# Kernel optimization log

Hardware: AMD Instinct MI355X
Metric: run time of the kernel (lower is better)

The kernel has to match this reference:

```python
import jax, jax.numpy as jnp
import numpy as np

T, B, D, H, S = 512, 32, 1024, 1024, 512


def setup_inputs() -> dict:
    key = jax.random.key(0)
    ks = jax.random.split(key, 10)
    sc = 0.02
    return {
        "x": jax.random.normal(ks[0], (T, B, D), jnp.float32),
        "h0": jax.random.normal(ks[1], (B, H), jnp.float32),
        "c0": jax.random.normal(ks[2], (B, H), jnp.float32),
        "ctx": jax.random.normal(ks[3], (S, B, H), jnp.float32),
        # nn.Linear(input_size, 4*hidden_size) with bias
        "W_ih": jax.random.normal(ks[4], (4 * H, D), jnp.float32) * sc,
        "b_ih": jax.random.normal(ks[5], (4 * H,), jnp.float32) * sc,
        # nn.Linear(hidden_size, 4*hidden_size) with bias
        "W_hh": jax.random.normal(ks[6], (4 * H, H), jnp.float32) * sc,
        "b_hh": jax.random.normal(ks[7], (4 * H,), jnp.float32) * sc,
        # SoftDotAttention: linear_in (H->H, no bias), linear_out (2H->H, no bias)
        "W_in": jax.random.normal(ks[8], (H, H), jnp.float32) * sc,
        "W_out": jax.random.normal(ks[9], (H, 2 * H), jnp.float32) * sc,
    }


def reference(x, h0, c0, ctx, W_ih, b_ih, W_hh, b_hh, W_in, W_out):
    ctx_b = jnp.swapaxes(ctx, 0, 1)  # [B, S, H] (ctx.transpose(0,1))

    def step(carry, xt):
        hx, cx = carry
        gates = xt @ W_ih.T + b_ih + hx @ W_hh.T + b_hh  # [B, 4H]
        i, f, g, o = jnp.split(gates, 4, axis=1)
        cy = jax.nn.sigmoid(f) * cx + jax.nn.sigmoid(i) * jnp.tanh(g)
        hy = jax.nn.sigmoid(o) * jnp.tanh(cy)  # [B, H]
        # SoftDotAttention
        target = hy @ W_in.T  # [B, H]
        attn = jax.nn.softmax(jnp.einsum("bsh,bh->bs", ctx_b, target), axis=-1)
        wc = jnp.einsum("bs,bsh->bh", attn, ctx_b)  # weighted context
        h_tilde = jnp.tanh(jnp.concatenate([wc, hy], axis=1) @ W_out.T)
        return (h_tilde, cy), h_tilde

    (hT, cT), out = jax.lax.scan(step, (h0, c0), x)
    return out, hT, cT
```

## Files before the change

### kernel.cpp

```cpp
#include <hip/hip_runtime.h>
#include <hip/hip_bf16.h>
#include <cstdint>
#include <cstddef>

#define TT 512
#define BB 32
#define DD 1024
#define HH 1024
#define SS 512

typedef _Float16 f16x8 __attribute__((ext_vector_type(8)));
typedef _Float16 f16x4 __attribute__((ext_vector_type(4)));
typedef _Float16 f16x2 __attribute__((ext_vector_type(2)));
typedef float f32x4 __attribute__((ext_vector_type(4)));

__device__ __forceinline__ float sigm(float x) { return 1.0f / (1.0f + __expf(-x)); }
__device__ __forceinline__ float tanh_fast(float x) {
    return 1.0f - 2.0f / (__expf(2.0f * x) + 1.0f);
}
__device__ __forceinline__ f16x8 cvt8(const float* __restrict__ p) {
    float4 u = *(const float4*)p;
    float4 v = *(const float4*)(p + 4);
    f16x8 r;
    r[0] = (_Float16)u.x; r[1] = (_Float16)u.y; r[2] = (_Float16)u.z; r[3] = (_Float16)u.w;
    r[4] = (_Float16)v.x; r[5] = (_Float16)v.y; r[6] = (_Float16)v.z; r[7] = (_Float16)v.w;
    return r;
}

__device__ __forceinline__ void st_u32_coh(unsigned* p, unsigned v) {
    __hip_atomic_store(p, v, __ATOMIC_RELAXED, __HIP_MEMORY_SCOPE_AGENT);
}
__device__ __forceinline__ unsigned ld_u32_coh(const unsigned* p) {
    return __hip_atomic_load(p, __ATOMIC_RELAXED, __HIP_MEMORY_SCOPE_AGENT);
}
__device__ __forceinline__ f16x8 ld16_coh(const _Float16* p) {
    union { unsigned long long q[2]; f16x8 h; } u;
    u.q[0] = __hip_atomic_load((const unsigned long long*)p, __ATOMIC_RELAXED,
                               __HIP_MEMORY_SCOPE_AGENT);
    u.q[1] = __hip_atomic_load((const unsigned long long*)p + 1, __ATOMIC_RELAXED,
                               __HIP_MEMORY_SCOPE_AGENT);
    return u.h;
}

__global__ __launch_bounds__(256) void k_cvt(const float* __restrict__ s,
                                             _Float16* __restrict__ d, int n4) {
    for (int i = blockIdx.x * blockDim.x + threadIdx.x; i < n4; i += gridDim.x * blockDim.x) {
        float4 v = ((const float4*)s)[i];
        f16x4 h;
        h[0] = (_Float16)v.x; h[1] = (_Float16)v.y;
        h[2] = (_Float16)v.z; h[3] = (_Float16)v.w;
        ((f16x4*)d)[i] = h;
    }
}

__global__ void k_bias(const float* __restrict__ bih, const float* __restrict__ bhh,
                       float* __restrict__ bsum) {
    const int i = blockIdx.x * blockDim.x + threadIdx.x;
    if (i < 4 * HH) bsum[i] = bih[i] + bhh[i];
}

__global__ void k_init(const float* __restrict__ c0, float* __restrict__ cbuf) {
    const int i = blockIdx.x * blockDim.x + threadIdx.x;
    if (i < BB * HH) cbuf[i] = c0[i];
}

__global__ void k_zero(unsigned* __restrict__ p) {
    const int i = blockIdx.x * blockDim.x + threadIdx.x;
    if (i < 1024) p[i] = 0u;
}

__global__ void k_fin(const float* __restrict__ lasth, const float* __restrict__ cbuf,
                      float* __restrict__ hT, float* __restrict__ cT) {
    const int i = blockIdx.x * blockDim.x + threadIdx.x;
    if (i < BB * HH) {
        hT[i] = lasth[i];
        cT[i] = cbuf[i];
    }
}

__global__ __launch_bounds__(256) void k_pre(const float* __restrict__ x,
                                             const float* __restrict__ Wih,
                                             _Float16* __restrict__ gx) {
    const int wave = (blockIdx.x * blockDim.x + threadIdx.x) >> 6;
    const int lane = threadIdx.x & 63;
    const int m0 = (wave >> 6) * 64, n0 = (wave & 63) * 64;
    const int lm = lane & 15, q8 = (lane >> 4) * 8;

    f32x4 acc[4][4];
    #pragma unroll
    for (int i = 0; i < 4; ++i)
        #pragma unroll
        for (int j = 0; j < 4; ++j) acc[i][j] = (f32x4)0.0f;

    for (int k0 = 0; k0 < DD; k0 += 32) {
        f16x8 a[4], b[4];
        #pragma unroll
        for (int i = 0; i < 4; ++i)
            a[i] = cvt8(x + (size_t)(m0 + i * 16 + lm) * DD + k0 + q8);
        #pragma unroll
        for (int j = 0; j < 4; ++j)
            b[j] = cvt8(Wih + (size_t)(n0 + j * 16 + lm) * DD + k0 + q8);
        #pragma unroll
        for (int i = 0; i < 4; ++i)
            #pragma unroll
            for (int j = 0; j < 4; ++j)
                acc[i][j] = __builtin_amdgcn_mfma_f32_16x16x32_f16(a[i], b[j], acc[i][j], 0, 0, 0);
    }
    const int rq = (lane >> 4) * 4;
    #pragma unroll
    for (int i = 0; i < 4; ++i)
        #pragma unroll
        for (int j = 0; j < 4; ++j)
            #pragma unroll
            for (int r = 0; r < 4; ++r)
                gx[(size_t)(m0 + i * 16 + rq + r) * (4 * HH) + n0 + j * 16 + lm] =
                    (_Float16)acc[i][j][r];
}

__global__ __launch_bounds__(256) void k_trwin(const float* __restrict__ Win,
                                               _Float16* __restrict__ WinT) {
    __shared__ float tile[32][33];
    const int bx = blockIdx.x & 31, by = blockIdx.x >> 5;
    const int tx = threadIdx.x & 31, ty = threadIdx.x >> 5;
    #pragma unroll
    for (int r = 0; r < 4; ++r)
        tile[ty + r * 8][tx] = Win[(size_t)(by * 32 + ty + r * 8) * HH + bx * 32 + tx];
    __syncthreads();
    #pragma unroll
    for (int r = 0; r < 4; ++r)
        WinT[(size_t)(bx * 32 + ty + r * 8) * HH + by * 32 + tx] =
            (_Float16)tile[tx][ty + r * 8];
}

__global__ __launch_bounds__(256) void k_ctxw(const float* __restrict__ ctxf,
                                              const _Float16* __restrict__ WinT,
                                              _Float16* __restrict__ ctxW) {
    const int wave = (blockIdx.x * blockDim.x + threadIdx.x) >> 6;
    const int lane = threadIdx.x & 63;
    const int m0 = (wave >> 4) * 64, n0 = (wave & 15) * 64;
    const int lm = lane & 15, q8 = (lane >> 4) * 8;

    f32x4 acc[4][4];
    #pragma unroll
    for (int i = 0; i < 4; ++i)
        #pragma unroll
        for (int j = 0; j < 4; ++j) acc[i][j] = (f32x4)0.0f;

    for (int k0 = 0; k0 < HH; k0 += 32) {
        f16x8 a[4], b[4];
        #pragma unroll
        for (int i = 0; i < 4; ++i)
            a[i] = cvt8(ctxf + (size_t)(m0 + i * 16 + lm) * HH + k0 + q8);
        #pragma unroll
        for (int j = 0; j < 4; ++j)
            b[j] = *(const f16x8*)(WinT + (size_t)(n0 + j * 16 + lm) * HH + k0 + q8);
        #pragma unroll
        for (int i = 0; i < 4; ++i)
            #pragma unroll
            for (int j = 0; j < 4; ++j)
                acc[i][j] = __builtin_amdgcn_mfma_f32_16x16x32_f16(a[i], b[j], acc[i][j], 0, 0, 0);
    }
    const int rq = (lane >> 4) * 4;
    #pragma unroll
    for (int i = 0; i < 4; ++i)
        #pragma unroll
        for (int j = 0; j < 4; ++j)
            #pragma unroll
            for (int r = 0; r < 4; ++r)
                ctxW[(size_t)(m0 + i * 16 + rq + r) * HH + n0 + j * 16 + lm] =
                    (_Float16)acc[i][j][r];
}

__device__ __forceinline__ void gbar4(unsigned* __restrict__ flags, unsigned round) {
    __syncthreads();
    const int tid = threadIdx.x;
    if (tid == 0) {
        asm volatile("s_waitcnt vmcnt(0)" ::: "memory");
        st_u32_coh(&flags[blockIdx.x], round);
    }
    if (tid < 64) {
        int guard = 0;
        for (;;) {
            const unsigned a0 = ld_u32_coh(&flags[tid * 4 + 0]);
            const unsigned a1 = ld_u32_coh(&flags[tid * 4 + 1]);
            const unsigned a2 = ld_u32_coh(&flags[tid * 4 + 2]);
            const unsigned a3 = ld_u32_coh(&flags[tid * 4 + 3]);
            if (a0 >= round && a1 >= round && a2 >= round && a3 >= round) break;
            __builtin_amdgcn_s_sleep(1);
            if (++guard > (1 << 20)) break;
        }
    }
    __syncthreads();
}

__global__ __launch_bounds__(512, 1) void k_persist(
    const _Float16* __restrict__ x16,
    const _Float16* __restrict__ ctx_h,
    const _Float16* __restrict__ ctxW,
    const float* __restrict__ Whh,
    const float* __restrict__ Wih,
    const float* __restrict__ Wout,
    const float* __restrict__ bsum,
    float* __restrict__ cbuf,
    _Float16* __restrict__ h16,
    _Float16* __restrict__ hy16,
    _Float16* __restrict__ wc16,
    float* __restrict__ scores,
    float* __restrict__ out,
    unsigned* __restrict__ bar) {
    __shared__ __align__(16) _Float16 sWHH[16 * 1024];
    __shared__ __align__(16) _Float16 sWIH[16 * 1024];
    __shared__ __align__(16) _Float16 sWOUT[4 * 2048];
    __shared__ __align__(16) float sRED[4096];
    __shared__ float sSM[512];

    const int bid = blockIdx.x;
    const int tid = threadIdx.x;
    const int w = tid >> 6, lane = tid & 63;
    const int lm = lane & 15, q8 = (lane >> 4) * 8;
    const int j0 = bid * 4;

    for (int idx = tid; idx < 16 * 128; idx += 512) {
        const int p = idx >> 7, k8 = idx & 127;
        const int g = (p >> 2) * HH + j0 + (p & 3);
        const int dst = (p * 2048 + k8 * 16) ^ ((p & 7) << 4);
        *(f16x8*)((char*)sWHH + dst) = cvt8(Whh + (size_t)g * HH + k8 * 8);
        *(f16x8*)((char*)sWIH + dst) = cvt8(Wih + (size_t)g * DD + k8 * 8);
    }
    for (int idx = tid; idx < 4 * 256; idx += 512) {
        const int p = idx >> 8, k8 = idx & 255;
        *(f16x8*)((char*)sWOUT + ((p * 4096 + k8 * 16) ^ (p << 4))) =
            cvt8(Wout + (size_t)(j0 + p) * (2 * HH) + k8 * 8);
    }
    __syncthreads();

    unsigned round = 0;
    for (int t = 0; t < TT; ++t) {
        {
            const int kb = (w & 3) * 256;
            f32x4 acc0 = (f32x4)0.0f, acc1 = (f32x4)0.0f;
            if (w < 4) {
                #pragma unroll
                for (int kk = 0; kk < 256; kk += 32) {
                    const int k0 = kb + kk + q8;
                    f16x8 a0 = ld16_coh(h16 + (size_t)lm * HH + k0);
                    f16x8 a1 = ld16_coh(h16 + (size_t)(16 + lm) * HH + k0);
                    f16x8 bb = *(const f16x8*)((const char*)sWHH +
                                 ((lm * 2048 + k0 * 2) ^ ((lm & 7) << 4)));
                    acc0 = __builtin_amdgcn_mfma_f32_16x16x32_f16(a0, bb, acc0, 0, 0, 0);
                    acc1 = __builtin_amdgcn_mfma_f32_16x16x32_f16(a1, bb, acc1, 0, 0, 0);
                }
            } else {
                const _Float16* Xb = x16 + (size_t)t * (BB * DD);
                #pragma unroll
                for (int kk = 0; kk < 256; kk += 32) {
                    const int k0 = kb + kk + q8;
                    f16x8 a0 = *(const f16x8*)(Xb + (size_t)lm * DD + k0);
                    f16x8 a1 = *(const f16x8*)(Xb + (size_t)(16 + lm) * DD + k0);
                    f16x8 bb = *(const f16x8*)((const char*)sWIH +
                                 ((lm * 2048 + k0 * 2) ^ ((lm & 7) << 4)));
                    acc0 = __builtin_amdgcn_mfma_f32_16x16x32_f16(a0, bb, acc0, 0, 0, 0);
                    acc1 = __builtin_amdgcn_mfma_f32_16x16x32_f16(a1, bb, acc1, 0, 0, 0);
                }
            }
            ((f32x4*)sRED)[(w * 2 + 0) * 64 + lane] = acc0;
            ((f32x4*)sRED)[(w * 2 + 1) * 64 + lane] = acc1;
            __syncthreads();
            {
                const int b = tid >> 4, p = tid & 15;
                const int mt = b >> 4, bi = b & 15;
                const int ln = ((bi >> 2) << 4) | p, r = bi & 3;
                float gv = 0.0f;
                #pragma unroll
                for (int w2 = 0; w2 < 8; ++w2)
                    gv += sRED[((w2 * 2 + mt) * 64 + ln) * 4 + r];
                sSM[tid] = gv;
            }
            __syncthreads();
            if (tid < 64) {
                const int b = tid >> 1, cp = (tid & 1) * 2;
                union { _Float16 h[2]; unsigned u; } pk;
                #pragma unroll
                for (int cc = 0; cc < 2; ++cc) {
                    const int c = cp + cc, j = j0 + c;
                    const float gi = sSM[b * 16 + 0 + c] + bsum[j];
                    const float gf = sSM[b * 16 + 4 + c] + bsum[HH + j];
                    const float gg = sSM[b * 16 + 8 + c] + bsum[2 * HH + j];
                    const float go = sSM[b * 16 + 12 + c] + bsum[3 * HH + j];
                    const float cprev = cbuf[b * HH + j];
                    const float cy = sigm(gf) * cprev + sigm(gi) * tanh_fast(gg);
                    const float hv = sigm(go) * tanh_fast(cy);
                    cbuf[b * HH + j] = cy;
                    pk.h[cc] = (_Float16)hv;
                }
                st_u32_coh((unsigned*)(hy16 + (size_t)b * HH + j0 + cp), pk.u);
            }
        }
        ++round;
        gbar4(bar, round);

        {
            const int b = bid & 31, s0 = (bid >> 5) * 64;
            const _Float16* hrow = hy16 + (size_t)b * HH + lane * 16;
            const f16x8 hv0 = ld16_coh(hrow);
            const f16x8 hv1 = ld16_coh(hrow + 8);
            float hf[16];
            #pragma unroll
            for (int i = 0; i < 8; ++i) { hf[i] = (float)hv0[i]; hf[8 + i] = (float)hv1[i]; }
            #pragma unroll
            for (int i = 0; i < 8; ++i) {
                const int s = s0 + w * 8 + i;
                const _Float16* crow = ctxW + ((size_t)s * BB + b) * HH + lane * 16;
                const f16x8 c0 = *(const f16x8*)(crow);
                const f16x8 c1 = *(const f16x8*)(crow + 8);
                float sum = 0.0f;
                #pragma unroll
                for (int jj = 0; jj < 8; ++jj)
                    sum += hf[jj] * (float)c0[jj] + hf[8 + jj] * (float)c1[jj];
                #pragma unroll
                for (int off = 32; off > 0; off >>= 1) sum += __shfl_down(sum, off, 64);
                if (lane == 0)
                    st_u32_coh((unsigned*)(scores + b * SS + s), __float_as_uint(sum));
            }
        }
        ++round;
        gbar4(bar, round);

        {
            const int b = bid >> 3, h0 = (bid & 7) * 128;
            const float v = __uint_as_float(ld_u32_coh((const unsigned*)(scores + b * SS + tid)));
            float mx = v;
            #pragma unroll
            for (int off = 32; off > 0; off >>= 1) mx = fmaxf(mx, __shfl_xor(mx, off, 64));
            if (lane == 0) sRED[w] = mx;
            __syncthreads();
            mx = sRED[0];
            #pragma unroll
            for (int w2 = 1; w2 < 8; ++w2) mx = fmaxf(mx, sRED[w2]);
            const float e = __expf(v - mx);
            sSM[tid] = e;
            float ssum = e;
            #pragma unroll
            for (int off = 32; off > 0; off >>= 1) ssum += __shfl_xor(ssum, off, 64);
            if (lane == 0) sRED[8 + w] = ssum;
            __syncthreads();
            float tot = 0.0f;
            #pragma unroll
            for (int w2 = 0; w2 < 8; ++w2) tot += sRED[8 + w2];
            const float inv = 1.0f / tot;
            float a0 = 0.0f, a1 = 0.0f;
            const _Float16* cb = ctx_h + ((size_t)(w * 64) * BB + b) * HH + h0 + lane * 2;
            #pragma unroll 16
            for (int i = 0; i < 64; ++i) {
                const float aw = sSM[w * 64 + i];
                const f16x2 u = *(const f16x2*)(cb + (size_t)i * (BB * HH));
                a0 += aw * (float)u[0];
                a1 += aw * (float)u[1];
            }
            __syncthreads();
            sRED[(w * 64 + lane) * 2 + 0] = a0;
            sRED[(w * 64 + lane) * 2 + 1] = a1;
            __syncthreads();
            if (tid < 64) {
                const int ln = tid;
                float sv0 = 0.0f, sv1 = 0.0f;
                #pragma unroll
                for (int w2 = 0; w2 < 8; ++w2) {
                    sv0 += sRED[(w2 * 64 + ln) * 2 + 0];
                    sv1 += sRED[(w2 * 64 + ln) * 2 + 1];
                }
                union { _Float16 h[2]; unsigned u; } pk;
                pk.h[0] = (_Float16)(sv0 * inv);
                pk.h[1] = (_Float16)(sv1 * inv);
                st_u32_coh((unsigned*)(wc16 + (size_t)b * HH + h0 + ln * 2), pk.u);
            }
        }
        ++round;
        gbar4(bar, round);

        {
            const _Float16* Ab = (w < 4) ? wc16 : hy16;
            const int kb = (w & 3) * 256;
            const int koff = (w < 4) ? 0 : HH;
            const int pc = lm & 3;
            f32x4 acc0 = (f32x4)0.0f, acc1 = (f32x4)0.0f;
            #pragma unroll
            for (int kk = 0; kk < 256; kk += 32) {
                const int k0 = kb + kk + q8;
                f16x8 a0 = ld16_coh(Ab + (size_t)lm * HH + k0);
                f16x8 a1 = ld16_coh(Ab + (size_t)(16 + lm) * HH + k0);
                f16x8 bb = *(const f16x8*)((char*)sWOUT +
                             ((pc * 4096 + (koff + k0) * 2) ^ (pc << 4)));
                acc0 = __builtin_amdgcn_mfma_f32_16x16x32_f16(a0, bb, acc0, 0, 0, 0);
                acc1 = __builtin_amdgcn_mfma_f32_16x16x32_f16(a1, bb, acc1, 0, 0, 0);
            }
            ((f32x4*)sRED)[(w * 2 + 0) * 64 + lane] = acc0;
            ((f32x4*)sRED)[(w * 2 + 1) * 64 + lane] = acc1;
            __syncthreads();
            {
                const int b = tid >> 4, p = tid & 15;
                const int mt = b >> 4, bi = b & 15;
                const int ln = ((bi >> 2) << 4) | p, r = bi & 3;
                float v2 = 0.0f;
                #pragma unroll
                for (int w2 = 0; w2 < 8; ++w2)
                    v2 += sRED[((w2 * 2 + mt) * 64 + ln) * 4 + r];
                const float ht = tanh_fast(v2);
                if (p < 4) out[(size_t)t * (BB * HH) + b * HH + j0 + p] = ht;
                sSM[tid] = ht;
            }
            __syncthreads();
            if (tid < 64) {
                const int b2 = tid >> 1, pp = (tid & 1) * 2;
                union { _Float16 h[2]; unsigned u; } pk;
                pk.h[0] = (_Float16)sSM[b2 * 16 + pp];
                pk.h[1] = (_Float16)sSM[b2 * 16 + pp + 1];
                st_u32_coh((unsigned*)(h16 + (size_t)b2 * HH + j0 + pp), pk.u);
            }
        }
        ++round;
        gbar4(bar, round);
    }
}

__global__ __launch_bounds__(64) void k_step1(const float* __restrict__ hprev,
                                              const _Float16* __restrict__ Whh_h,
                                              const float* __restrict__ Whh_f,
                                              const _Float16* __restrict__ gx_t,
                                              const float* __restrict__ xt_f,
                                              const _Float16* __restrict__ Wih_h,
                                              const float* __restrict__ Wih_f,
                                              const float* __restrict__ bsum,
                                              float* __restrict__ cbuf,
                                              float* __restrict__ hy,
                                              int use_pre, int staged) {
    const int wave = blockIdx.x;
    const int lane = threadIdx.x;
    const int m0 = (wave >> 6) * 16;
    const int j0 = (wave & 63) * 16;
    const int lm = lane & 15, q8 = (lane >> 4) * 8;

    f32x4 acc[4];
    #pragma unroll
    for (int q = 0; q < 4; ++q) acc[q] = (f32x4)0.0f;

    const float* arow = hprev + (size_t)(m0 + lm) * HH;
    if (staged) {
        for (int k0 = 0; k0 < HH; k0 += 32) {
            f16x8 a = cvt8(arow + k0 + q8);
            #pragma unroll
            for (int q = 0; q < 4; ++q) {
                f16x8 b = *(const f16x8*)(Whh_h + (size_t)(q * HH + j0 + lm) * HH + k0 + q8);
                acc[q] = __builtin_amdgcn_mfma_f32_16x16x32_f16(a, b, acc[q], 0, 0, 0);
            }
        }
    } else {
        for (int k0 = 0; k0 < HH; k0 += 32) {
            f16x8 a = cvt8(arow + k0 + q8);
            #pragma unroll
            for (int q = 0; q < 4; ++q) {
                f16x8 b = cvt8(Whh_f + (size_t)(q * HH + j0 + lm) * HH + k0 + q8);
                acc[q] = __builtin_amdgcn_mfma_f32_16x16x32_f16(a, b, acc[q], 0, 0, 0);
            }
        }
    }
    if (!use_pre) {
        const float* xrow = xt_f + (size_t)(m0 + lm) * DD;
        if (staged) {
            for (int k0 = 0; k0 < DD; k0 += 32) {
                f16x8 a = cvt8(xrow + k0 + q8);
                #pragma unroll
                for (int q = 0; q < 4; ++q) {
                    f16x8 b = *(const f16x8*)(Wih_h + (size_t)(q * HH + j0 + lm) * DD + k0 + q8);
                    acc[q] = __builtin_amdgcn_mfma_f32_16x16x32_f16(a, b, acc[q], 0, 0, 0);
                }
            }
        } else {
            for (int k0 = 0; k0 < DD; k0 += 32) {
                f16x8 a = cvt8(xrow + k0 + q8);
                #pragma unroll
                for (int q = 0; q < 4; ++q) {
                    f16x8 b = cvt8(Wih_f + (size_t)(q * HH + j0 + lm) * DD + k0 + q8);
                    acc[q] = __builtin_amdgcn_mfma_f32_16x16x32_f16(a, b, acc[q], 0, 0, 0);
                }
            }
        }
    }
    const int rq = (lane >> 4) * 4;
    const int j = j0 + lm;
    const float bs_i = bsum[j], bs_f = bsum[HH + j], bs_g = bsum[2 * HH + j], bs_o = bsum[3 * HH + j];
    #pragma unroll
    for (int r = 0; r < 4; ++r) {
        const int b = m0 + rq + r;
        float gi = acc[0][r] + bs_i, gf = acc[1][r] + bs_f;
        float gg = acc[2][r] + bs_g, go = acc[3][r] + bs_o;
        if (use_pre) {
            const _Float16* g = gx_t + (size_t)b * (4 * HH);
            gi += (float)g[j];
            gf += (float)g[HH + j];
            gg += (float)g[2 * HH + j];
            go += (float)g[3 * HH + j];
        }
        const float cprev = cbuf[b * HH + j];
        const float cy = sigm(gf) * cprev + sigm(gi) * tanh_fast(gg);
        const float hv = sigm(go) * tanh_fast(cy);
        cbuf[b * HH + j] = cy;
        hy[b * HH + j] = hv;
    }
}

__global__ __launch_bounds__(64) void k_target(const float* __restrict__ hy,
                                               const _Float16* __restrict__ Win_h,
                                               const float* __restrict__ Win_f,
                                               float* __restrict__ target,
                                               int staged) {
    const int wave = blockIdx.x;
    const int lane = threadIdx.x;
    const int m0 = (wave >> 6) * 16;
    const int j0 = (wave & 63) * 16;
    const int lm = lane & 15, q8 = (lane >> 4) * 8;

    f32x4 acc = (f32x4)0.0f;
    const float* arow = hy + (size_t)(m0 + lm) * HH;
    if (staged) {
        for (int k0 = 0; k0 < HH; k0 += 32) {
            f16x8 a = cvt8(arow + k0 + q8);
            f16x8 b = *(const f16x8*)(Win_h + (size_t)(j0 + lm) * HH + k0 + q8);
            acc = __builtin_amdgcn_mfma_f32_16x16x32_f16(a, b, acc, 0, 0, 0);
        }
    } else {
        for (int k0 = 0; k0 < HH; k0 += 32) {
            f16x8 a = cvt8(arow + k0 + q8);
            f16x8 b = cvt8(Win_f + (size_t)(j0 + lm) * HH + k0 + q8);
            acc = __builtin_amdgcn_mfma_f32_16x16x32_f16(a, b, acc, 0, 0, 0);
        }
    }
    const int rq = (lane >> 4) * 4;
    const int j = j0 + lm;
    #pragma unroll
    for (int r = 0; r < 4; ++r)
        target[(m0 + rq + r) * HH + j] = acc[r];
}

__global__ __launch_bounds__(256) void k_scores(const _Float16* __restrict__ ctx_h,
                                                const float* __restrict__ ctx_f,
                                                const float* __restrict__ target,
                                                float* __restrict__ scores, int staged) {
    const int idx = (blockIdx.x * blockDim.x + threadIdx.x) >> 6;
    const int lane = threadIdx.x & 63;
    const int b = idx >> 9;
    const int s = idx & 511;
    const float* trow = target + b * HH + lane * 16;
    float4 t0 = *(const float4*)(trow);
    float4 t1 = *(const float4*)(trow + 4);
    float4 t2 = *(const float4*)(trow + 8);
    float4 t3 = *(const float4*)(trow + 12);
    float sum = 0.0f;
    if (staged) {
        const _Float16* crow = ctx_h + ((size_t)s * BB + b) * HH + lane * 16;
        f16x8 c0 = *(const f16x8*)(crow);
        f16x8 c1 = *(const f16x8*)(crow + 8);
        sum += (float)c0[0] * t0.x + (float)c0[1] * t0.y + (float)c0[2] * t0.z + (float)c0[3] * t0.w;
        sum += (float)c0[4] * t1.x + (float)c0[5] * t1.y + (float)c0[6] * t1.z + (float)c0[7] * t1.w;
        sum += (float)c1[0] * t2.x + (float)c1[1] * t2.y + (float)c1[2] * t2.z + (float)c1[3] * t2.w;
        sum += (float)c1[4] * t3.x + (float)c1[5] * t3.y + (float)c1[6] * t3.z + (float)c1[7] * t3.w;
    } else {
        const float* crow = ctx_f + ((size_t)s * BB + b) * HH + lane * 16;
        float4 c0 = *(const float4*)(crow);
        float4 c1 = *(const float4*)(crow + 4);
        float4 c2 = *(const float4*)(crow + 8);
        float4 c3 = *(const float4*)(crow + 12);
        sum += c0.x * t0.x + c0.y * t0.y + c0.z * t0.z + c0.w * t0.w;
        sum += c1.x * t1.x + c1.y * t1.y + c1.z * t1.z + c1.w * t1.w;
        sum += c2.x * t2.x + c2.y * t2.y + c2.z * t2.z + c2.w * t2.w;
        sum += c3.x * t3.x + c3.y * t3.y + c3.z * t3.z + c3.w * t3.w;
    }
    #pragma unroll
    for (int off = 32; off > 0; off >>= 1) sum += __shfl_down(sum, off, 64);
    if (lane == 0) scores[b * SS + s] = sum;
}

__global__ __launch_bounds__(256) void k_attn(const _Float16* __restrict__ ctx_h,
                                              const float* __restrict__ ctx_f,
                                              const float* __restrict__ scores,
                                              float* __restrict__ wc, int staged) {
    __shared__ float sm[SS];
    __shared__ float red[256];
    const int b = blockIdx.x >> 1;
    const int hc = blockIdx.x & 1;
    const int t = threadIdx.x;

    const float v0 = scores[b * SS + t];
    const float v1 = scores[b * SS + 256 + t];
    red[t] = fmaxf(v0, v1);
    __syncthreads();
    for (int o = 128; o > 0; o >>= 1) {
        if (t < o) red[t] = fmaxf(red[t], red[t + o]);
        __syncthreads();
    }
    const float mx = red[0];
    __syncthreads();
    const float e0 = __expf(v0 - mx);
    const float e1 = __expf(v1 - mx);
    sm[t] = e0;
    sm[t + 256] = e1;
    red[t] = e0 + e1;
    __syncthreads();
    for (int o = 128; o > 0; o >>= 1) {
        if (t < o) red[t] += red[t + o];
        __syncthreads();
    }
    const float inv = 1.0f / red[0];

    const int h = hc * 512 + t * 2;
    float a0 = 0.0f, a1 = 0.0f;
    if (staged) {
        const _Float16* cbase = ctx_h + (size_t)b * HH + h;
        #pragma unroll 8
        for (int s = 0; s < SS; ++s) {
            const float a = sm[s];
            const f16x2 u = *(const f16x2*)(cbase + (size_t)s * (BB * HH));
            a0 += a * (float)u[0];
            a1 += a * (float)u[1];
        }
    } else {
        const float* cbase = ctx_f + (size_t)b * HH + h;
        #pragma unroll 8
        for (int s = 0; s < SS; ++s) {
            const float a = sm[s];
            const float2 u = *(const float2*)(cbase + (size_t)s * (BB * HH));
            a0 += a * u.x;
            a1 += a * u.y;
        }
    }
    wc[b * HH + h] = a0 * inv;
    wc[b * HH + h + 1] = a1 * inv;
}

__global__ __launch_bounds__(64) void k_out(const float* __restrict__ wc,
                                            const float* __restrict__ hy,
                                            const _Float16* __restrict__ Wout_h,
                                            const float* __restrict__ Wout_f,
                                            float* __restrict__ out_t,
                                            int staged) {
    const int wave = blockIdx.x;
    const int lane = threadIdx.x;
    const int m0 = (wave >> 6) * 16;
    const int j0 = (wave & 63) * 16;
    const int lm = lane & 15, q8 = (lane >> 4) * 8;

    f32x4 acc = (f32x4)0.0f;
    const float* arow1 = wc + (size_t)(m0 + lm) * HH;
    const float* arow2 = hy + (size_t)(m0 + lm) * HH;
    if (staged) {
        const _Float16* brow = Wout_h + (size_t)(j0 + lm) * (2 * HH);
        for (int k0 = 0; k0 < HH; k0 += 32) {
            f16x8 a = cvt8(arow1 + k0 + q8);
            f16x8 b = *(const f16x8*)(brow + k0 + q8);
            acc = __builtin_amdgcn_mfma_f32_16x16x32_f16(a, b, acc, 0, 0, 0);
        }
        for (int k0 = 0; k0 < HH; k0 += 32) {
            f16x8 a = cvt8(arow2 + k0 + q8);
            f16x8 b = *(const f16x8*)(brow + HH + k0 + q8);
            acc = __builtin_amdgcn_mfma_f32_16x16x32_f16(a, b, acc, 0, 0, 0);
        }
    } else {
        const float* brow = Wout_f + (size_t)(j0 + lm) * (2 * HH);
        for (int k0 = 0; k0 < HH; k0 += 32) {
            f16x8 a = cvt8(arow1 + k0 + q8);
            f16x8 b = cvt8(brow + k0 + q8);
            acc = __builtin_amdgcn_mfma_f32_16x16x32_f16(a, b, acc, 0, 0, 0);
        }
        for (int k0 = 0; k0 < HH; k0 += 32) {
            f16x8 a = cvt8(arow2 + k0 + q8);
            f16x8 b = cvt8(brow + HH + k0 + q8);
            acc = __builtin_amdgcn_mfma_f32_16x16x32_f16(a, b, acc, 0, 0, 0);
        }
    }
    const int rq = (lane >> 4) * 4;
    const int j = j0 + lm;
    #pragma unroll
    for (int r = 0; r < 4; ++r)
        out_t[(m0 + rq + r) * HH + j] = tanh_fast(acc[r]);
}

static constexpr size_t NW_CBUF   = 0;
static constexpr size_t NW_SCORES = 131072;
static constexpr size_t NW_HY16   = 196608;
static constexpr size_t NW_H16    = 262144;
static constexpr size_t NW_WC16   = 327680;
static constexpr size_t NW_BSUM   = 393216;
static constexpr size_t NW_BAR    = 409600;
static constexpr size_t NW_WINT   = 413696;
static constexpr size_t NW_X16    = 2510848;
static constexpr size_t NW_CTXH   = 36065280;
static constexpr size_t NW_CTXW   = 69619712;
static constexpr size_t NW_TOTAL  = 103174144;

extern "C" void kernel_launch(void* const* d_in, const int* in_sizes, int n_in,
                              void* d_out, int out_size, void* d_ws, size_t ws_size,
                              hipStream_t stream) {
    const float* x    = (const float*)d_in[0];
    const float* h0   = (const float*)d_in[1];
    const float* c0   = (const float*)d_in[2];
    const float* ctx  = (const float*)d_in[3];
    const float* Wih  = (const float*)d_in[4];
    const float* bih  = (const float*)d_in[5];
    const float* Whh  = (const float*)d_in[6];
    const float* bhh  = (const float*)d_in[7];
    const float* Win  = (const float*)d_in[8];
    const float* Wout = (const float*)d_in[9];
    float* out = (float*)d_out;
    char* ws = (char*)d_ws;

    if (ws_size >= NW_TOTAL) {
        float* cbuf       = (float*)(ws + NW_CBUF);
        float* scores     = (float*)(ws + NW_SCORES);
        _Float16* hy16    = (_Float16*)(ws + NW_HY16);
        _Float16* h16     = (_Float16*)(ws + NW_H16);
        _Float16* wc16    = (_Float16*)(ws + NW_WC16);
        float* bsum       = (float*)(ws + NW_BSUM);
        unsigned* bar     = (unsigned*)(ws + NW_BAR);
        _Float16* WinT    = (_Float16*)(ws + NW_WINT);
        _Float16* x16     = (_Float16*)(ws + NW_X16);
        _Float16* ctx_h   = (_Float16*)(ws + NW_CTXH);
        _Float16* ctxW    = (_Float16*)(ws + NW_CTXW);

        k_bias<<<16, 256, 0, stream>>>(bih, bhh, bsum);
        k_init<<<128, 256, 0, stream>>>(c0, cbuf);
        k_zero<<<4, 256, 0, stream>>>(bar);
        k_cvt<<<2048, 256, 0, stream>>>(ctx, ctx_h, SS * BB * HH / 4);
        k_cvt<<<4096, 256, 0, stream>>>(x, x16, TT * BB * DD / 4);
        k_cvt<<<32, 256, 0, stream>>>(h0, h16, BB * HH / 4);
        k_trwin<<<1024, 256, 0, stream>>>(Win, WinT);
        k_ctxw<<<1024, 256, 0, stream>>>(ctx, WinT, ctxW);

        k_persist<<<256, 512, 0, stream>>>(x16, ctx_h, ctxW, Whh, Wih, Wout, bsum,
                                           cbuf, h16, hy16, wc16, scores, out, bar);

        float* hT = out + (size_t)TT * BB * HH;
        float* cT = hT + BB * HH;
        k_fin<<<128, 256, 0, stream>>>(out + (size_t)(TT - 1) * BB * HH, cbuf, hT, cT);
        return;
    }

    float* cbuf   = (float*)(ws + 0);
    float* hy     = (float*)(ws + 131072);
    float* target = (float*)(ws + 262144);
    float* scores = (float*)(ws + 393216);
    float* wc     = (float*)(ws + 458752);
    float* bsum   = (float*)(ws + 589824);
    _Float16* Whh_h  = (_Float16*)(ws + 606208);
    _Float16* Win_h  = (_Float16*)(ws + 8994816);
    _Float16* Wout_h = (_Float16*)(ws + 11091968);
    _Float16* Wih_h  = (_Float16*)(ws + 15286272);
    _Float16* ctx_h  = (_Float16*)(ws + 23674880);
    _Float16* gx     = (_Float16*)(ws + 57229312);

    const int staged  = (ws_size >= (size_t)57229312) ? 1 : 0;
    const int use_pre = (ws_size >= (size_t)191447040) ? 1 : 0;

    k_bias<<<16, 256, 0, stream>>>(bih, bhh, bsum);
    k_init<<<128, 256, 0, stream>>>(c0, cbuf);
    if (staged) {
        k_cvt<<<1024, 256, 0, stream>>>(Whh, Whh_h, 4 * HH * HH / 4);
        k_cvt<<<1024, 256, 0, stream>>>(Win, Win_h, HH * HH / 4);
        k_cvt<<<1024, 256, 0, stream>>>(Wout, Wout_h, 2 * HH * HH / 4);
        k_cvt<<<2048, 256, 0, stream>>>(ctx, ctx_h, SS * BB * HH / 4);
        if (!use_pre) k_cvt<<<1024, 256, 0, stream>>>(Wih, Wih_h, 4 * HH * DD / 4);
    }
    if (use_pre) k_pre<<<4096, 256, 0, stream>>>(x, Wih, gx);

    for (int t = 0; t < TT; ++t) {
        const float* hprev = (t == 0) ? h0 : (out + (size_t)(t - 1) * BB * HH);
        const _Float16* gx_t = gx + (size_t)t * BB * 4 * HH;
        const float* xt = x + (size_t)t * BB * DD;
        float* out_t = out + (size_t)t * BB * HH;

        k_step1<<<128, 64, 0, stream>>>(hprev, Whh_h, Whh, gx_t, xt, Wih_h, Wih,
                                        bsum, cbuf, hy, use_pre, staged);
        k_target<<<128, 64, 0, stream>>>(hy, Win_h, Win, target, staged);
        k_scores<<<4096, 256, 0, stream>>>(ctx_h, ctx, target, scores, staged);
        k_attn<<<64, 256, 0, stream>>>(ctx_h, ctx, scores, wc, staged);
        k_out<<<128, 64, 0, stream>>>(wc, hy, Wout_h, Wout, out_t, staged);
    }

    float* hT = out + (size_t)TT * BB * HH;
    float* cT = hT + BB * HH;
    k_fin<<<128, 256, 0, stream>>>(out + (size_t)(TT - 1) * BB * HH, cbuf, hT, cT);
}
```

Baseline: 22.62 ms.

## Use acquire fence in grid barrier, plain loads, register-resident cell state, vectorized attention

Replaces the per-load agent-scope atomic loads of shared activations with plain vector loads, and adds an acquire fence after the grid barrier spin to keep them correct. Keeps the LSTM cell state in shared memory across timesteps instead of round-tripping through global memory, writing it back once at the end. Also batches the context loads in the score computation and widens the weighted-context reduction to 8-wide f16 loads with cross-lane shuffles. The aim is lower per-step latency in the persistent kernel, at the cost of relying on the fence for visibility of plain loads.

After: 23.70 ms. 1.05x slower.

```diff
diff --git a/kernel.cpp b/kernel.cpp
--- a/kernel.cpp
+++ b/kernel.cpp
@@ -32,14 +32,6 @@
 }
 __device__ __forceinline__ unsigned ld_u32_coh(const unsigned* p) {
     return __hip_atomic_load(p, __ATOMIC_RELAXED, __HIP_MEMORY_SCOPE_AGENT);
-}
-__device__ __forceinline__ f16x8 ld16_coh(const _Float16* p) {
-    union { unsigned long long q[2]; f16x8 h; } u;
-    u.q[0] = __hip_atomic_load((const unsigned long long*)p, __ATOMIC_RELAXED,
-                               __HIP_MEMORY_SCOPE_AGENT);
-    u.q[1] = __hip_atomic_load((const unsigned long long*)p + 1, __ATOMIC_RELAXED,
-                               __HIP_MEMORY_SCOPE_AGENT);
-    return u.h;
 }
 
 __global__ __launch_bounds__(256) void k_cvt(const float* __restrict__ s,
@@ -171,7 +163,7 @@
                     (_Float16)acc[i][j][r];
 }
 
-__device__ __forceinline__ void gbar4(unsigned* __restrict__ flags, unsigned round) {
+__device__ __forceinline__ void gbar5(unsigned* __restrict__ flags, unsigned round) {
     __syncthreads();
     const int tid = threadIdx.x;
     if (tid == 0) {
@@ -189,6 +181,7 @@
             __builtin_amdgcn_s_sleep(1);
             if (++guard > (1 << 20)) break;
         }
+        __builtin_amdgcn_fence(__ATOMIC_ACQUIRE, "agent");
     }
     __syncthreads();
 }
@@ -201,6 +194,7 @@
     const float* __restrict__ Wih,
     const float* __restrict__ Wout,
     const float* __restrict__ bsum,
+    const float* __restrict__ c0i,
     float* __restrict__ cbuf,
     _Float16* __restrict__ h16,
     _Float16* __restrict__ hy16,
@@ -213,6 +207,7 @@
     __shared__ __align__(16) _Float16 sWOUT[4 * 2048];
     __shared__ __align__(16) float sRED[4096];
     __shared__ float sSM[512];
+    __shared__ float sCB[128];
 
     const int bid = blockIdx.x;
     const int tid = threadIdx.x;
@@ -232,6 +227,7 @@
         *(f16x8*)((char*)sWOUT + ((p * 4096 + k8 * 16) ^ (p << 4))) =
             cvt8(Wout + (size_t)(j0 + p) * (2 * HH) + k8 * 8);
     }
+    if (tid < 128) sCB[tid] = c0i[(size_t)(tid >> 2) * HH + j0 + (tid & 3)];
     __syncthreads();
 
     unsigned round = 0;
@@ -243,8 +239,8 @@
                 #pragma unroll
                 for (int kk = 0; kk < 256; kk += 32) {
                     const int k0 = kb + kk + q8;
-                    f16x8 a0 = ld16_coh(h16 + (size_t)lm * HH + k0);
-                    f16x8 a1 = ld16_coh(h16 + (size_t)(16 + lm) * HH + k0);
+                    f16x8 a0 = *(const f16x8*)(h16 + (size_t)lm * HH + k0);
+                    f16x8 a1 = *(const f16x8*)(h16 + (size_t)(16 + lm) * HH + k0);
                     f16x8 bb = *(const f16x8*)((const char*)sWHH +
                                  ((lm * 2048 + k0 * 2) ^ ((lm & 7) << 4)));
                     acc0 = __builtin_amdgcn_mfma_f32_16x16x32_f16(a0, bb, acc0, 0, 0, 0);
@@ -287,48 +283,53 @@
                     const float gf = sSM[b * 16 + 4 + c] + bsum[HH + j];
                     const float gg = sSM[b * 16 + 8 + c] + bsum[2 * HH + j];
                     const float go = sSM[b * 16 + 12 + c] + bsum[3 * HH + j];
-                    const float cprev = cbuf[b * HH + j];
+                    const float cprev = sCB[b * 4 + c];
                     const float cy = sigm(gf) * cprev + sigm(gi) * tanh_fast(gg);
                     const float hv = sigm(go) * tanh_fast(cy);
-                    cbuf[b * HH + j] = cy;
+                    sCB[b * 4 + c] = cy;
                     pk.h[cc] = (_Float16)hv;
                 }
                 st_u32_coh((unsigned*)(hy16 + (size_t)b * HH + j0 + cp), pk.u);
             }
         }
         ++round;
-        gbar4(bar, round);
+        gbar5(bar, round);
 
         {
             const int b = bid & 31, s0 = (bid >> 5) * 64;
             const _Float16* hrow = hy16 + (size_t)b * HH + lane * 16;
-            const f16x8 hv0 = ld16_coh(hrow);
-            const f16x8 hv1 = ld16_coh(hrow + 8);
+            const f16x8 hv0 = *(const f16x8*)(hrow);
+            const f16x8 hv1 = *(const f16x8*)(hrow + 8);
             float hf[16];
             #pragma unroll
             for (int i = 0; i < 8; ++i) { hf[i] = (float)hv0[i]; hf[8 + i] = (float)hv1[i]; }
+            f16x8 cr0[8], cr1[8];
             #pragma unroll
             for (int i = 0; i < 8; ++i) {
-                const int s = s0 + w * 8 + i;
-                const _Float16* crow = ctxW + ((size_t)s * BB + b) * HH + lane * 16;
-                const f16x8 c0 = *(const f16x8*)(crow);
-                const f16x8 c1 = *(const f16x8*)(crow + 8);
+                const _Float16* crow =
+                    ctxW + ((size_t)(s0 + w * 8 + i) * BB + b) * HH + lane * 16;
+                cr0[i] = *(const f16x8*)(crow);
+                cr1[i] = *(const f16x8*)(crow + 8);
+            }
+            #pragma unroll
+            for (int i = 0; i < 8; ++i) {
                 float sum = 0.0f;
                 #pragma unroll
                 for (int jj = 0; jj < 8; ++jj)
-                    sum += hf[jj] * (float)c0[jj] + hf[8 + jj] * (float)c1[jj];
+                    sum += hf[jj] * (float)cr0[i][jj] + hf[8 + jj] * (float)cr1[i][jj];
                 #pragma unroll
                 for (int off = 32; off > 0; off >>= 1) sum += __shfl_down(sum, off, 64);
                 if (lane == 0)
-                    st_u32_coh((unsigned*)(scores + b * SS + s), __float_as_uint(sum));
+                    st_u32_coh((unsigned*)(scores + b * SS + s0 + w * 8 + i),
+                               __float_as_uint(sum));
             }
         }
         ++round;
-        gbar4(bar, round);
+        gbar5(bar, round);
 
         {
             const int b = bid >> 3, h0 = (bid & 7) * 128;
-            const float v = __uint_as_float(ld_u32_coh((const unsigned*)(scores + b * SS + tid)));
+            const float v = scores[b * SS + tid];
             float mx = v;
             #pragma unroll
             for (int off = 32; off > 0; off >>= 1) mx = fmaxf(mx, __shfl_xor(mx, off, 64));
@@ -348,35 +349,46 @@
             #pragma unroll
             for (int w2 = 0; w2 < 8; ++w2) tot += sRED[8 + w2];
             const float inv = 1.0f / tot;
-            float a0 = 0.0f, a1 = 0.0f;
-            const _Float16* cb = ctx_h + ((size_t)(w * 64) * BB + b) * HH + h0 + lane * 2;
-            #pragma unroll 16
-            for (int i = 0; i < 64; ++i) {
-                const float aw = sSM[w * 64 + i];
-                const f16x2 u = *(const f16x2*)(cb + (size_t)i * (BB * HH));
-                a0 += aw * (float)u[0];
-                a1 += aw * (float)u[1];
+            const int g = lane >> 4, c = lane & 15;
+            float acc[8];
+            #pragma unroll
+            for (int j = 0; j < 8; ++j) acc[j] = 0.0f;
+            const _Float16* cb =
+                ctx_h + ((size_t)(w * 64 + g) * BB + b) * HH + h0 + c * 8;
+            #pragma unroll
+            for (int i = 0; i < 16; ++i) {
+                const float aw = sSM[w * 64 + g + i * 4];
+                const f16x8 u = *(const f16x8*)(cb + (size_t)(i * 4) * (BB * HH));
+                #pragma unroll
+                for (int j = 0; j < 8; ++j) acc[j] += aw * (float)u[j];
+            }
+            #pragma unroll
+            for (int j = 0; j < 8; ++j) {
+                acc[j] += __shfl_xor(acc[j], 16, 64);
+                acc[j] += __shfl_xor(acc[j], 32, 64);
             }
             __syncthreads();
-            sRED[(w * 64 + lane) * 2 + 0] = a0;
-            sRED[(w * 64 + lane) * 2 + 1] = a1;
+            if (g == 0) {
+                #pragma unroll
+                for (int j = 0; j < 8; ++j) sRED[w * 128 + c * 8 + j] = acc[j];
+            }
             __syncthreads();
             if (tid < 64) {
-                const int ln = tid;
+                const int cc = tid * 2;
                 float sv0 = 0.0f, sv1 = 0.0f;
                 #pragma unroll
                 for (int w2 = 0; w2 < 8; ++w2) {
-                    sv0 += sRED[(w2 * 64 + ln) * 2 + 0];
-                    sv1 += sRED[(w2 * 64 + ln) * 2 + 1];
+                    sv0 += sRED[w2 * 128 + cc];
+                    sv1 += sRED[w2 * 128 + cc + 1];
                 }
                 union { _Float16 h[2]; unsigned u; } pk;
                 pk.h[0] = (_Float16)(sv0 * inv);
                 pk.h[1] = (_Float16)(sv1 * inv);
-                st_u32_coh((unsigned*)(wc16 + (size_t)b * HH + h0 + ln * 2), pk.u);
+                st_u32_coh((unsigned*)(wc16 + (size_t)b * HH + h0 + cc), pk.u);
             }
         }
         ++round;
-        gbar4(bar, round);
+        gbar5(bar, round);
 
         {
             const _Float16* Ab = (w < 4) ? wc16 : hy16;
@@ -387,8 +399,8 @@
             #pragma unroll
             for (int kk = 0; kk < 256; kk += 32) {
                 const int k0 = kb + kk + q8;
-                f16x8 a0 = ld16_coh(Ab + (size_t)lm * HH + k0);
-                f16x8 a1 = ld16_coh(Ab + (size_t)(16 + lm) * HH + k0);
+                f16x8 a0 = *(const f16x8*)(Ab + (size_t)lm * HH + k0);
+                f16x8 a1 = *(const f16x8*)(Ab + (size_t)(16 + lm) * HH + k0);
                 f16x8 bb = *(const f16x8*)((char*)sWOUT +
                              ((pc * 4096 + (koff + k0) * 2) ^ (pc << 4)));
                 acc0 = __builtin_amdgcn_mfma_f32_16x16x32_f16(a0, bb, acc0, 0, 0, 0);
@@ -406,7 +418,9 @@
                 for (int w2 = 0; w2 < 8; ++w2)
                     v2 += sRED[((w2 * 2 + mt) * 64 + ln) * 4 + r];
                 const float ht = tanh_fast(v2);
-                if (p < 4) out[(size_t)t * (BB * HH) + b * HH + j0 + p] = ht;
+                if (p < 4)
+                    st_u32_coh((unsigned*)(out + (size_t)t * (BB * HH) + b * HH + j0 + p),
+                               __float_as_uint(ht));
                 sSM[tid] = ht;
             }
             __syncthreads();
@@ -419,8 +433,12 @@
             }
         }
         ++round;
-        gbar4(bar, round);
-    }
+        gbar5(bar, round);
+    }
+
+    if (tid < 128)
+        st_u32_coh((unsigned*)&cbuf[(size_t)(tid >> 2) * HH + j0 + (tid & 3)],
+                   __float_as_uint(sCB[tid]));
 }
 
 __global__ __launch_bounds__(64) void k_step1(const float* __restrict__ hprev,
@@ -727,7 +745,6 @@
         _Float16* ctxW    = (_Float16*)(ws + NW_CTXW);
 
         k_bias<<<16, 256, 0, stream>>>(bih, bhh, bsum);
-        k_init<<<128, 256, 0, stream>>>(c0, cbuf);
         k_zero<<<4, 256, 0, stream>>>(bar);
         k_cvt<<<2048, 256, 0, stream>>>(ctx, ctx_h, SS * BB * HH / 4);
         k_cvt<<<4096, 256, 0, stream>>>(x, x16, TT * BB * DD / 4);
@@ -736,7 +753,7 @@
         k_ctxw<<<1024, 256, 0, stream>>>(ctx, WinT, ctxW);
 
         k_persist<<<256, 512, 0, stream>>>(x16, ctx_h, ctxW, Whh, Wih, Wout, bsum,
-                                           cbuf, h16, hy16, wc16, scores, out, bar);
+                                           c0, cbuf, h16, hy16, wc16, scores, out, bar);
 
         float* hT = out + (size_t)TT * BB * HH;
         float* cT = hT + BB * HH;
```
